# Kernel tuning notes

Measured on AMD Instinct MI355X. Metric: run time of the kernel, lower is better.

The kernel has to match this reference:

```python
import jax, jax.numpy as jnp
import numpy as np

# Per-channel block sizes (matches init_kwargs):
#   channels  0:16  -> block (1,1)  (plain ReLU)
#   channels 16:40  -> block (2,2)
#   channels 40:56  -> block (3,3)  (needs padding for H=W=256)
#   channels 56:64  -> identity (block contains 0)
GROUPS = [(0, 16, 1, 1), (16, 40, 2, 2), (40, 56, 3, 3)]  # (ch_start, ch_end, b0, b1)


def setup_inputs() -> dict:
    key = jax.random.key(0)
    activation = jax.random.normal(key, (16, 64, 256, 256), dtype=jnp.float32)
    return {"activation": activation}


def _group_mask(x, b0, b1):
    # x: [N, Cg, H, W] -> DReLU of per-block sum, broadcast back to [N, Cg, H, W]
    N, Cg, H, W = x.shape
    pr = (-H) % b0
    pc = (-W) % b1
    xp = jnp.pad(x, ((0, 0), (0, 0), (0, pr), (0, pc)))
    Hp, Wp = H + pr, W + pc
    blocks = xp.reshape(N, Cg, Hp // b0, b0, Wp // b1, b1)
    s = blocks.sum(axis=(3, 5))                      # [N, Cg, Hp/b0, Wp/b1] block sums
    sign = (s >= 0).astype(x.dtype)                  # DReLU
    mask = jnp.broadcast_to(
        sign[:, :, :, None, :, None], (N, Cg, Hp // b0, b0, Wp // b1, b1)
    ).reshape(N, Cg, Hp, Wp)
    return mask[:, :, :H, :W]                        # unpad


def reference(activation):
    out = activation
    for cs, ce, b0, b1 in GROUPS:
        x = activation[:, cs:ce]
        mask = _group_mask(x, b0, b1)
        out = out.at[:, cs:ce].set(x * mask)
    # identity channels (56:64) stay untouched
    return out
```

## Files before the change

kernel.cpp:

```cpp
#include <hip/hip_runtime.h>


static constexpr int W = 256;
static constexpr int HWP = 256 * 256;

__global__ __launch_bounds__(256) void k_elem(const float* __restrict__ in,
                                              float* __restrict__ out) {
    int t = blockIdx.x * 256 + threadIdx.x;
    int plane = t >> 14;
    int off   = t & 16383;
    int n  = plane / 24;
    int cc = plane - n * 24;
    int c  = (cc < 16) ? cc : cc + 40;
    int idx = (n * 64 + c) * (HWP / 4) + off;
    float4 v = reinterpret_cast<const float4*>(in)[idx];
    if (cc < 16) {
        v.x = (v.x >= 0.f) ? v.x : 0.f;
        v.y = (v.y >= 0.f) ? v.y : 0.f;
        v.z = (v.z >= 0.f) ? v.z : 0.f;
        v.w = (v.w >= 0.f) ? v.w : 0.f;
    }
    reinterpret_cast<float4*>(out)[idx] = v;
}

__global__ __launch_bounds__(256) void k_b2(const float* __restrict__ in,
                                            float* __restrict__ out) {
    int t = blockIdx.x * 256 + threadIdx.x;
    int plane = t >> 13;
    int off   = t & 8191;
    int brow  = off >> 6;
    int q     = off & 63;
    int n  = plane / 24;
    int cc = plane - n * 24;
    int base = (n * 64 + cc + 16) * HWP + brow * 2 * W + q * 4;
    float4 a = *reinterpret_cast<const float4*>(in + base);
    float4 b = *reinterpret_cast<const float4*>(in + base + W);
    float s0 = ((a.x + a.y) + b.x) + b.y;
    float s1 = ((a.z + a.w) + b.z) + b.w;
    if (s0 < 0.f) { a.x = 0.f; a.y = 0.f; b.x = 0.f; b.y = 0.f; }
    if (s1 < 0.f) { a.z = 0.f; a.w = 0.f; b.z = 0.f; b.w = 0.f; }
    *reinterpret_cast<float4*>(out + base)     = a;
    *reinterpret_cast<float4*>(out + base + W) = b;
}

__global__ __launch_bounds__(256) void k_b3(const float* __restrict__ in,
                                            float* __restrict__ out) {
    int t = blockIdx.x * 256 + threadIdx.x;
    int plane = t / 7396;
    int off   = t - plane * 7396;
    int brow  = off / 86;
    int bcol  = off - brow * 86;
    int n = plane >> 4;
    int c = 40 + (plane & 15);
    int r0 = brow * 3;
    int c0 = bcol * 3;
    bool rv = (brow < 85);
    bool cv = (bcol < 85);
    const float* p = in + (n * 64 + c) * HWP + r0 * W + c0;
    float v00 = p[0];
    float v01 = cv ? p[1] : 0.f;
    float v02 = cv ? p[2] : 0.f;
    float v10 = rv ? p[W + 0] : 0.f;
    float v11 = (rv && cv) ? p[W + 1] : 0.f;
    float v12 = (rv && cv) ? p[W + 2] : 0.f;
    float v20 = rv ? p[2 * W + 0] : 0.f;
    float v21 = (rv && cv) ? p[2 * W + 1] : 0.f;
    float v22 = (rv && cv) ? p[2 * W + 2] : 0.f;
    float s = v00;
    s += v01; s += v02;
    s += v10; s += v11; s += v12;
    s += v20; s += v21; s += v22;
    if (s < 0.f) {
        v00 = v01 = v02 = v10 = v11 = v12 = v20 = v21 = v22 = 0.f;
    }
    float* q = out + (n * 64 + c) * HWP + r0 * W + c0;
    q[0] = v00;
    if (cv) { q[1] = v01; q[2] = v02; }
    if (rv) {
        q[W] = v10;
        if (cv) { q[W + 1] = v11; q[W + 2] = v12; }
        q[2 * W] = v20;
        if (cv) { q[2 * W + 1] = v21; q[2 * W + 2] = v22; }
    }
}

extern "C" void kernel_launch(void* const* d_in, const int* in_sizes, int n_in,
                              void* d_out, int out_size, void* d_ws, size_t ws_size,
                              hipStream_t stream) {
    const float* in = (const float*)d_in[0];
    float* out = (float*)d_out;

    k_elem<<<24576, 256, 0, stream>>>(in, out);
    k_b2<<<12288, 256, 0, stream>>>(in, out);
    k_b3<<<7396, 256, 0, stream>>>(in, out);
}
```

Measured before the change: 430.9 us.

## Fuse three block-ReLU kernels into one launch with LDS-staged 3x3 path

Merges the elementwise, 2x2 and 3x3 kernels into a single launch that dispatches on block index ranges. The 3x3 path now has each workgroup load one 3-row strip with coalesced float4 loads into shared memory, compute per-block signs with 86 threads, and write the masked rows back as float4. This is meant to remove the uncoalesced scalar access of the old 3x3 kernel and the overhead between launches. In exchange it adds two barriers and leaves many threads idle during the reduction.

```diff
diff --git a/kernel.cpp b/kernel.cpp
--- a/kernel.cpp
+++ b/kernel.cpp
@@ -1,86 +1,97 @@
 #include <hip/hip_runtime.h>
 
 
-static constexpr int W = 256;
+static constexpr int W   = 256;
 static constexpr int HWP = 256 * 256;
 
-__global__ __launch_bounds__(256) void k_elem(const float* __restrict__ in,
-                                              float* __restrict__ out) {
-    int t = blockIdx.x * 256 + threadIdx.x;
-    int plane = t >> 14;
-    int off   = t & 16383;
-    int n  = plane / 24;
-    int cc = plane - n * 24;
-    int c  = (cc < 16) ? cc : cc + 40;
-    int idx = (n * 64 + c) * (HWP / 4) + off;
-    float4 v = reinterpret_cast<const float4*>(in)[idx];
-    if (cc < 16) {
-        v.x = (v.x >= 0.f) ? v.x : 0.f;
-        v.y = (v.y >= 0.f) ? v.y : 0.f;
-        v.z = (v.z >= 0.f) ? v.z : 0.f;
-        v.w = (v.w >= 0.f) ? v.w : 0.f;
+static constexpr int NB_ELEM = 24576;
+static constexpr int NB_B2   = 12288;
+static constexpr int NB_B3   = 22016;
+
+__global__ __launch_bounds__(256) void fused_blockrelu(const float* __restrict__ in,
+                                                       float* __restrict__ out) {
+    __shared__ float lds[3 * W];
+    __shared__ float msk[86];
+    int b   = blockIdx.x;
+    int tid = threadIdx.x;
+
+    if (b < NB_ELEM) {
+        int t     = b * 256 + tid;
+        int plane = t >> 14;
+        int off   = t & 16383;
+        int n  = plane / 24;
+        int cc = plane - n * 24;
+        int c  = (cc < 16) ? cc : cc + 40;
+        int idx = (n * 64 + c) * (HWP / 4) + off;
+        float4 v = reinterpret_cast<const float4*>(in)[idx];
+        if (cc < 16) {
+            v.x = (v.x >= 0.f) ? v.x : 0.f;
+            v.y = (v.y >= 0.f) ? v.y : 0.f;
+            v.z = (v.z >= 0.f) ? v.z : 0.f;
+            v.w = (v.w >= 0.f) ? v.w : 0.f;
+        }
+        reinterpret_cast<float4*>(out)[idx] = v;
+        return;
     }
-    reinterpret_cast<float4*>(out)[idx] = v;
-}
+    b -= NB_ELEM;
 
-__global__ __launch_bounds__(256) void k_b2(const float* __restrict__ in,
-                                            float* __restrict__ out) {
-    int t = blockIdx.x * 256 + threadIdx.x;
-    int plane = t >> 13;
-    int off   = t & 8191;
-    int brow  = off >> 6;
-    int q     = off & 63;
-    int n  = plane / 24;
-    int cc = plane - n * 24;
-    int base = (n * 64 + cc + 16) * HWP + brow * 2 * W + q * 4;
-    float4 a = *reinterpret_cast<const float4*>(in + base);
-    float4 b = *reinterpret_cast<const float4*>(in + base + W);
-    float s0 = ((a.x + a.y) + b.x) + b.y;
-    float s1 = ((a.z + a.w) + b.z) + b.w;
-    if (s0 < 0.f) { a.x = 0.f; a.y = 0.f; b.x = 0.f; b.y = 0.f; }
-    if (s1 < 0.f) { a.z = 0.f; a.w = 0.f; b.z = 0.f; b.w = 0.f; }
-    *reinterpret_cast<float4*>(out + base)     = a;
-    *reinterpret_cast<float4*>(out + base + W) = b;
-}
+    if (b < NB_B2) {
+        int t     = b * 256 + tid;
+        int plane = t >> 13;
+        int off   = t & 8191;
+        int brow  = off >> 6;
+        int q     = off & 63;
+        int n  = plane / 24;
+        int cc = plane - n * 24;
+        int base = (n * 64 + cc + 16) * HWP + brow * 2 * W + q * 4;
+        float4 a = *reinterpret_cast<const float4*>(in + base);
+        float4 c4 = *reinterpret_cast<const float4*>(in + base + W);
+        float s0 = ((a.x + a.y) + c4.x) + c4.y;
+        float s1 = ((a.z + a.w) + c4.z) + c4.w;
+        if (s0 < 0.f) { a.x = 0.f; a.y = 0.f; c4.x = 0.f; c4.y = 0.f; }
+        if (s1 < 0.f) { a.z = 0.f; a.w = 0.f; c4.z = 0.f; c4.w = 0.f; }
+        *reinterpret_cast<float4*>(out + base)     = a;
+        *reinterpret_cast<float4*>(out + base + W) = c4;
+        return;
+    }
+    b -= NB_B2;
 
-__global__ __launch_bounds__(256) void k_b3(const float* __restrict__ in,
-                                            float* __restrict__ out) {
-    int t = blockIdx.x * 256 + threadIdx.x;
-    int plane = t / 7396;
-    int off   = t - plane * 7396;
-    int brow  = off / 86;
-    int bcol  = off - brow * 86;
+    int rb    = b % 86;
+    int plane = b / 86;
     int n = plane >> 4;
     int c = 40 + (plane & 15);
-    int r0 = brow * 3;
-    int c0 = bcol * 3;
-    bool rv = (brow < 85);
-    bool cv = (bcol < 85);
-    const float* p = in + (n * 64 + c) * HWP + r0 * W + c0;
-    float v00 = p[0];
-    float v01 = cv ? p[1] : 0.f;
-    float v02 = cv ? p[2] : 0.f;
-    float v10 = rv ? p[W + 0] : 0.f;
-    float v11 = (rv && cv) ? p[W + 1] : 0.f;
-    float v12 = (rv && cv) ? p[W + 2] : 0.f;
-    float v20 = rv ? p[2 * W + 0] : 0.f;
-    float v21 = (rv && cv) ? p[2 * W + 1] : 0.f;
-    float v22 = (rv && cv) ? p[2 * W + 2] : 0.f;
-    float s = v00;
-    s += v01; s += v02;
-    s += v10; s += v11; s += v12;
-    s += v20; s += v21; s += v22;
-    if (s < 0.f) {
-        v00 = v01 = v02 = v10 = v11 = v12 = v20 = v21 = v22 = 0.f;
+    const float* pin  = in  + (n * 64 + c) * HWP;
+    float*       pout = out + (n * 64 + c) * HWP;
+    int r0    = rb * 3;
+    int nrows = (rb < 85) ? 3 : 1;
+    int row = tid >> 6;
+    int q   = tid & 63;
+
+    if (row < nrows) {
+        float4 v = *reinterpret_cast<const float4*>(pin + (r0 + row) * W + q * 4);
+        *reinterpret_cast<float4*>(&lds[row * W + q * 4]) = v;
     }
-    float* q = out + (n * 64 + c) * HWP + r0 * W + c0;
-    q[0] = v00;
-    if (cv) { q[1] = v01; q[2] = v02; }
-    if (rv) {
-        q[W] = v10;
-        if (cv) { q[W + 1] = v11; q[W + 2] = v12; }
-        q[2 * W] = v20;
-        if (cv) { q[2 * W + 1] = v21; q[2 * W + 2] = v22; }
+    __syncthreads();
+
+    if (tid < 86) {
+        int c0    = tid * 3;
+        int ncols = (tid < 85) ? 3 : 1;
+        float s = 0.f;
+        for (int r = 0; r < nrows; ++r)
+            for (int k = 0; k < ncols; ++k)
+                s += lds[r * W + c0 + k];
+        msk[tid] = (s >= 0.f) ? 1.f : 0.f;
+    }
+    __syncthreads();
+
+    if (row < nrows) {
+        int c0 = q * 4;
+        float4 v = *reinterpret_cast<float4*>(&lds[row * W + c0]);
+        v.x *= msk[(c0 + 0) / 3];
+        v.y *= msk[(c0 + 1) / 3];
+        v.z *= msk[(c0 + 2) / 3];
+        v.w *= msk[(c0 + 3) / 3];
+        *reinterpret_cast<float4*>(pout + (r0 + row) * W + c0) = v;
     }
 }
 
@@ -89,8 +100,5 @@
                               hipStream_t stream) {
     const float* in = (const float*)d_in[0];
     float* out = (float*)d_out;
-
-    k_elem<<<24576, 256, 0, stream>>>(in, out);
-    k_b2<<<12288, 256, 0, stream>>>(in, out);
-    k_b3<<<7396, 256, 0, stream>>>(in, out);
+    fused_blockrelu<<<NB_ELEM + NB_B2 + NB_B3, 256, 0, stream>>>(in, out);
 }
```

Measured after the change: 425.6 us. Within noise of the previous version (-1.2%).
